# Optimization experiments

Hardware: AMD Instinct MI355X
Metric: run time of the kernel (lower is better)

## Reference

```python
import jax, jax.numpy as jnp
import numpy as np

R = 64  # all tensor-ring ranks equal

def setup_inputs() -> dict:
    key = jax.random.key(0)
    k1, k2, k3 = jax.random.split(key, 3)
    B, T, N, M, C = 512, 64, 512, 64, 100
    # xavier-uniform-ish scale for weights (gain=init_value=1.0)
    s_sh = float(np.sqrt(6.0 / (R * N + R)))
    s_la = float(np.sqrt(6.0 / (C * R * M + R)))
    return {
        "tensor": jax.random.normal(k1, (B, T, N), dtype=jnp.float32),
        "W_shared": jax.random.uniform(k2, (R, N, R), dtype=jnp.float32, minval=-s_sh, maxval=s_sh),
        "W_last": jax.random.uniform(k3, (C, R, M, R), dtype=jnp.float32, minval=-s_la, maxval=s_la),
    }

def reference(tensor, W_shared, W_last):
    B = tensor.shape[0]
    xt = jnp.transpose(tensor, (1, 0, 2))  # [T, B, N]
    state0 = jnp.ones((R, B, R), dtype=tensor.dtype)  # [r1, B, r2]
    # per-step: x = einsum('bj,rbi->rbji'); state = einsum('ijk,rbji->rbk')
    # == einsum('bj,rbi,ijk->rbk'); factored to avoid the [r,b,n,r] intermediate
    def step(state, x_t):
        bik = jnp.einsum('bj,ijk->bik', x_t, W_shared)   # [B, r2, r3]
        new = jnp.einsum('rbi,bik->rbk', state, bik)     # [r1, B, r3]
        return new, None
    state, _ = jax.lax.scan(step, state0, xt)
    # last kernel with pad_input = ones(B, m):
    # einsum('cijk,rbji->cbrk') with x[r,b,j,i]=state[r,b,i] == sum over j of W_last
    W_sum = jnp.sum(W_last, axis=2)                      # [C, r2, r_last]
    state = jnp.einsum('cik,rbi->cbrk', W_sum, state)    # [C, B, r1, r_last]
    # trace over the last two (square) rank dims
    out = jnp.einsum('cbrr->cb', state)                  # [C, B]
    return out
```

## Files before the change

kernel.cpp:

```cpp
#include <hip/hip_runtime.h>
#include <hip/hip_fp16.h>


typedef _Float16 f16;
typedef __attribute__((ext_vector_type(8))) _Float16 f16x8;
typedef __attribute__((ext_vector_type(2))) _Float16 f16x2;
typedef __attribute__((ext_vector_type(4))) float f32x4;

#define GLDS16(g, l)                                                      \
    __builtin_amdgcn_global_load_lds(                                     \
        (const __attribute__((address_space(1))) void*)(g),               \
        (__attribute__((address_space(3))) void*)(l), 16, 0, 0)

#define BARRIER() asm volatile("s_barrier" ::: "memory")
#define VMCNT(n) asm volatile("s_waitcnt vmcnt(" #n ")" ::: "memory")
#define WAVE_LDS_FENCE()                                                  \
    do {                                                                  \
        asm volatile("s_waitcnt lgkmcnt(0)" ::: "memory");                \
        __builtin_amdgcn_sched_barrier(0);                                \
    } while (0)

__global__ __launch_bounds__(256) void k_usum(const float* __restrict__ Wl,
                                              float* __restrict__ u) {
    int ci = blockIdx.x;
    const float4* p = (const float4*)(Wl + (size_t)ci * 4096);
    int tid = threadIdx.x;
    float s = 0.f;
#pragma unroll
    for (int q = 0; q < 4; ++q) {
        float4 v = p[tid + 256 * q];
        s += v.x + v.y + v.z + v.w;
    }
    __shared__ float red[256];
    red[tid] = s;
    __syncthreads();
    if (tid < 128) red[tid] += red[tid + 128];
    __syncthreads();
    if (tid < 64) {
        float x = red[tid] + red[tid + 64];
#pragma unroll
        for (int off = 32; off > 0; off >>= 1) x += __shfl_down(x, off, 64);
        if (tid == 0) u[ci] = x;
    }
}

__global__ __launch_bounds__(256) void k_prep(const float* __restrict__ tensor,
                                              const float* __restrict__ Wsh,
                                              const float* __restrict__ Wl,
                                              f16* __restrict__ Af16,
                                              f16* __restrict__ Btw,
                                              float* __restrict__ u) {
    __shared__ float red[256];
    int blk = blockIdx.x;
    int tid = threadIdx.x;
    if (blk < 8192) {
        int idx = blk * 256 + tid;
        const float4* p = (const float4*)tensor + (size_t)idx * 2;
        float4 v0 = p[0], v1 = p[1];
        f16x8 h;
        h[0] = (f16)v0.x; h[1] = (f16)v0.y; h[2] = (f16)v0.z; h[3] = (f16)v0.w;
        h[4] = (f16)v1.x; h[5] = (f16)v1.y; h[6] = (f16)v1.z; h[7] = (f16)v1.w;
        *(f16x8*)(Af16 + (size_t)idx * 8) = h;
    } else if (blk < 12288) {
        int o = (blk - 8192) * 256 + tid;
        int col = o >> 8;
        int j = (o & 255) << 1;
        int k = col >> 6, i = col & 63;
        const float* src = Wsh + ((size_t)i * 512 + j) * 64 + k;
        f16x2 pk;
        pk[0] = (f16)src[0];
        pk[1] = (f16)src[64];
        *(f16x2*)(Btw + (size_t)col * 512 + j) = pk;
    } else {
        int ci = blk - 12288;
        const float4* p = (const float4*)(Wl + (size_t)ci * 4096);
        float s = 0.f;
#pragma unroll
        for (int q = 0; q < 4; ++q) {
            float4 v = p[tid + 256 * q];
            s += v.x + v.y + v.z + v.w;
        }
        red[tid] = s;
        __syncthreads();
        if (tid < 128) red[tid] += red[tid + 128];
        __syncthreads();
        if (tid < 64) {
            float x = red[tid] + red[tid + 64];
#pragma unroll
            for (int off = 32; off > 0; off >>= 1) x += __shfl_down(x, off, 64);
            if (tid == 0) u[ci] = x;
        }
    }
}

#define STAGE_A(qq, ha, ktv) do {                                             \
    _Pragma("unroll") for (int u_ = 0; u_ < 2; ++u_) {                        \
        int idx_ = (wid * 2 + u_) * 64 + lane;                                \
        int r_ = idx_ >> 3;                                                   \
        int ls_ = (idx_ & 7) ^ (r_ & 7);                                      \
        const f16* g_ = A + (size_t)(m0 + (ha) * 128 + r_) * 512              \
                          + (ktv) * 64 + ls_ * 8;                             \
        char* l_ = smem + (qq) * 65536 + (ha) * 16384 + (wid * 2 + u_) * 1024;\
        GLDS16(g_, l_);                                                       \
    } } while (0)

#define STAGE_B(qq, hb, ktv) do {                                             \
    _Pragma("unroll") for (int u_ = 0; u_ < 2; ++u_) {                        \
        int idx_ = (wid * 2 + u_) * 64 + lane;                                \
        int r_ = idx_ >> 3;                                                   \
        int ls_ = (idx_ & 7) ^ (r_ & 7);                                      \
        const f16* g_ = Bt + (size_t)(n0 + (hb) * 128 + r_) * 512             \
                           + (ktv) * 64 + ls_ * 8;                            \
        char* l_ = smem + (qq) * 65536 + 32768 + (hb) * 16384                 \
                        + (wid * 2 + u_) * 1024;                              \
        GLDS16(g_, l_);                                                       \
    } } while (0)

#define RD_A(ha, ktv) do {                                                    \
    _Pragma("unroll") for (int mf_ = 0; mf_ < 4; ++mf_)                       \
    _Pragma("unroll") for (int kq_ = 0; kq_ < 2; ++kq_) {                     \
        int ra_ = wr * 64 + mf_ * 16 + (lane & 15);                           \
        int off_ = ((ra_ << 7) + kq_ * 64 + ((lane >> 4) << 4))               \
                   ^ ((ra_ & 7) << 4);                                        \
        a[mf_][kq_] = *(const f16x8*)(smem + ((ktv) & 1) * 65536              \
                                      + (ha) * 16384 + off_);                 \
    } } while (0)

#define RD_B(hb, ktv, breg) do {                                              \
    _Pragma("unroll") for (int nf_ = 0; nf_ < 2; ++nf_)                       \
    _Pragma("unroll") for (int kq_ = 0; kq_ < 2; ++kq_) {                     \
        int rb_ = wc * 32 + nf_ * 16 + (lane & 15);                           \
        int off_ = ((rb_ << 7) + kq_ * 64 + ((lane >> 4) << 4))               \
                   ^ ((rb_ & 7) << 4);                                        \
        breg[nf_][kq_] = *(const f16x8*)(smem + ((ktv) & 1) * 65536           \
                                         + 32768 + (hb) * 16384 + off_);      \
    } } while (0)

#define MFMA_Q(qa_, qb_, breg) do {                                           \
    __builtin_amdgcn_s_setprio(1);                                            \
    _Pragma("unroll") for (int mf_ = 0; mf_ < 4; ++mf_)                       \
    _Pragma("unroll") for (int nf_ = 0; nf_ < 2; ++nf_)                       \
    _Pragma("unroll") for (int kq_ = 0; kq_ < 2; ++kq_)                       \
        acc[qa_][qb_][mf_][nf_] = __builtin_amdgcn_mfma_f32_16x16x32_f16(     \
            a[mf_][kq_], breg[nf_][kq_], acc[qa_][qb_][mf_][nf_], 0, 0, 0);   \
    __builtin_amdgcn_s_setprio(0);                                            \
    } while (0)

__global__ __launch_bounds__(512) void k_gemm_256(const f16* __restrict__ A,
                                                  const f16* __restrict__ Bt,
                                                  __half* __restrict__ outp) {
    extern __shared__ char smem[];
    const int tid = threadIdx.x;
    const int lane = tid & 63;
    const int wid = tid >> 6;
    int lin = blockIdx.x;
    int swz = (lin & 7) * 256 + (lin >> 3);
    const int n0 = (swz & 15) * 256;
    const int m0 = (swz >> 4) * 256;
    const int wr = wid >> 2, wc = wid & 3;

    f32x4 acc[2][2][4][2];
#pragma unroll
    for (int x = 0; x < 2; ++x)
#pragma unroll
        for (int y = 0; y < 2; ++y)
#pragma unroll
            for (int z = 0; z < 4; ++z)
#pragma unroll
                for (int w = 0; w < 2; ++w) acc[x][y][z][w] = (f32x4)0.f;

    f16x8 a[4][2], b0[2][2], b1[2][2];

    STAGE_A(0, 0, 0);
    STAGE_B(0, 0, 0);
    STAGE_B(0, 1, 0);
    STAGE_A(0, 1, 0);
    STAGE_A(1, 0, 1);
    STAGE_B(1, 0, 1);
    STAGE_B(1, 1, 1);

    for (int kt = 0; kt < 6; ++kt) {
        VMCNT(6);
        BARRIER();
        RD_A(0, kt);
        RD_B(0, kt, b0);
        STAGE_A((kt + 1) & 1, 1, kt + 1);
        MFMA_Q(0, 0, b0);
        BARRIER();
        RD_B(1, kt, b1);
        MFMA_Q(0, 1, b1);
        BARRIER();
        RD_A(1, kt);
        STAGE_A(kt & 1, 0, kt + 2);
        STAGE_B(kt & 1, 0, kt + 2);
        MFMA_Q(1, 0, b0);
        BARRIER();
        STAGE_B(kt & 1, 1, kt + 2);
        MFMA_Q(1, 1, b1);
        BARRIER();
    }
    {
        VMCNT(6);
        BARRIER();
        RD_A(0, 6);
        RD_B(0, 6, b0);
        STAGE_A(1, 1, 7);
        MFMA_Q(0, 0, b0);
        BARRIER();
        RD_B(1, 6, b1);
        MFMA_Q(0, 1, b1);
        BARRIER();
        RD_A(1, 6);
        MFMA_Q(1, 0, b0);
        BARRIER();
        MFMA_Q(1, 1, b1);
        BARRIER();
    }
    {
        VMCNT(0);
        BARRIER();
        RD_A(0, 7);
        RD_B(0, 7, b0);
        MFMA_Q(0, 0, b0);
        BARRIER();
        RD_B(1, 7, b1);
        MFMA_Q(0, 1, b1);
        BARRIER();
        RD_A(1, 7);
        MFMA_Q(1, 0, b0);
        BARRIER();
        MFMA_Q(1, 1, b1);
        BARRIER();
    }

    __half* Cs = (__half*)smem;
#pragma unroll
    for (int qa = 0; qa < 2; ++qa)
#pragma unroll
        for (int qb = 0; qb < 2; ++qb)
#pragma unroll
            for (int mf = 0; mf < 4; ++mf)
#pragma unroll
                for (int nf = 0; nf < 2; ++nf)
#pragma unroll
                    for (int j = 0; j < 4; ++j) {
                        int row = qa * 128 + wr * 64 + mf * 16 + ((lane >> 4) << 2) + j;
                        int col = qb * 128 + wc * 32 + nf * 16 + (lane & 15);
                        Cs[row * 256 + col] = __float2half(acc[qa][qb][mf][nf][j]);
                    }
    BARRIER();
#pragma unroll
    for (int it = 0; it < 16; ++it) {
        int idx = it * 512 + tid;
        int r = idx >> 5, seg = idx & 31;
        __builtin_nontemporal_store(
            *(const f32x4*)(Cs + r * 256 + seg * 8),
            (f32x4*)(outp + (size_t)(m0 + r) * 4096 + n0 + seg * 8));
    }
}

#define BM 128
#define BN 64
#define BK 32
__global__ __launch_bounds__(256) void k_gemm(const float* __restrict__ A,
                                              const float* __restrict__ W,
                                              __half* __restrict__ out,
                                              int a_off, int a_stride) {
    __shared__ float As[BK * BM];
    __shared__ float Bs[BK * BN];
    int i0 = blockIdx.x;
    int m0 = blockIdx.y * BM;
    int tid = threadIdx.x;
    int tx = tid & 15, ty = tid >> 4;
    float acc[8][4];
#pragma unroll
    for (int q = 0; q < 8; ++q)
#pragma unroll
        for (int c = 0; c < 4; ++c) acc[q][c] = 0.f;
    const float* wbase = W + (size_t)i0 * 32768;
    for (int j0 = 0; j0 < 512; j0 += BK) {
        {
            int c4 = tid & 7;
            int r = tid >> 3;
#pragma unroll
            for (int p = 0; p < 4; ++p) {
                int row = r + 32 * p;
                float4 v = *(const float4*)(A + (size_t)a_off +
                                            (size_t)(m0 + row) * a_stride + j0 + 4 * c4);
                As[(4 * c4 + 0) * BM + row] = v.x;
                As[(4 * c4 + 1) * BM + row] = v.y;
                As[(4 * c4 + 2) * BM + row] = v.z;
                As[(4 * c4 + 3) * BM + row] = v.w;
            }
            const float4* src = (const float4*)(wbase + (size_t)j0 * 64);
            float4* dst = (float4*)Bs;
            dst[tid] = src[tid];
            dst[tid + 256] = src[tid + 256];
        }
        __syncthreads();
#pragma unroll
        for (int kk = 0; kk < BK; ++kk) {
            float bv[4], av[8];
#pragma unroll
            for (int c = 0; c < 4; ++c) bv[c] = Bs[kk * BN + 4 * tx + c];
#pragma unroll
            for (int q = 0; q < 8; ++q) av[q] = As[kk * BM + 8 * ty + q];
#pragma unroll
            for (int q = 0; q < 8; ++q)
#pragma unroll
                for (int c = 0; c < 4; ++c) acc[q][c] += av[q] * bv[c];
        }
        __syncthreads();
    }
#pragma unroll
    for (int q = 0; q < 8; ++q) {
        int m = m0 + 8 * ty + q;
        __half* o = out + (size_t)m * 4096 + i0 * 64 + 4 * tx;
#pragma unroll
        for (int c = 0; c < 4; ++c) o[c] = __float2half(acc[q][c]);
    }
}

__global__ __launch_bounds__(128) void k_scan_t(const __half* __restrict__ bik,
                                                const float* __restrict__ u,
                                                float* __restrict__ out) {
    __shared__ float vsh[2][64];
    const int tid = threadIdx.x;
    const int wid = tid >> 6;
    const int k = tid & 63;
    const int b = blockIdx.x * 2 + wid;
    float* vs = vsh[wid];
    const f16* row = (const f16*)bik + ((size_t)b * 64) * 4096 + k * 64;

    vs[k] = 1.0f;
    f16x8 A0[8], A1[8];
#pragma unroll
    for (int q = 0; q < 8; ++q) A0[q] = *(const f16x8*)(row + q * 8);
#pragma unroll
    for (int q = 0; q < 8; ++q) A1[q] = *(const f16x8*)(row + 4096 + q * 8);
    WAVE_LDS_FENCE();

#define SCAN_T_STEP(BUF, tnext) do {                                          \
    float s0 = 0.f, s1 = 0.f, s2 = 0.f, s3 = 0.f;                             \
    _Pragma("unroll") for (int q_ = 0; q_ < 8; q_ += 4) {                     \
        _Pragma("unroll") for (int e_ = 0; e_ < 8; ++e_) {                    \
            s0 += vs[(q_ + 0) * 8 + e_] * (float)BUF[q_ + 0][e_];             \
            s1 += vs[(q_ + 1) * 8 + e_] * (float)BUF[q_ + 1][e_];             \
            s2 += vs[(q_ + 2) * 8 + e_] * (float)BUF[q_ + 2][e_];             \
            s3 += vs[(q_ + 3) * 8 + e_] * (float)BUF[q_ + 3][e_];             \
        }                                                                     \
    }                                                                         \
    if ((tnext) < 64) {                                                       \
        const f16* r_ = row + (size_t)(tnext) * 4096;                         \
        _Pragma("unroll") for (int q_ = 0; q_ < 8; ++q_)                      \
            BUF[q_] = *(const f16x8*)(r_ + q_ * 8);                           \
    }                                                                         \
    vs[k] = (s0 + s1) + (s2 + s3);                                            \
    WAVE_LDS_FENCE();                                                         \
    } while (0)

    for (int t = 0; t < 64; t += 2) {
        SCAN_T_STEP(A0, t + 2);
        SCAN_T_STEP(A1, t + 3);
    }

    for (int c = k; c < 100; c += 64) {
        const float* uc = u + c * 64;
        float s = 0.f;
#pragma unroll 8
        for (int i = 0; i < 64; ++i) s += uc[i] * vs[i];
        out[c * 512 + b] = s;
    }
}

__global__ __launch_bounds__(256) void k_scan(const __half* __restrict__ bik,
                                              const float* __restrict__ u,
                                              float* __restrict__ out) {
    __shared__ char sm[2][8192];
    __shared__ float vsh[64];
    __shared__ float part[256];
    int b = blockIdx.x;
    int tid = threadIdx.x;
    int k = tid & 63, grp = tid >> 6;
    const int lane = tid & 63;
    const int wid = tid >> 6;
    if (tid < 64) vsh[tid] = 1.0f;
    const char* base = (const char*)(bik + (size_t)b * 64 * 4096);
#pragma unroll
    for (int u_ = 0; u_ < 2; ++u_) {
        const char* g = base + (wid * 2 + u_) * 1024 + lane * 16;
        GLDS16(g, &sm[0][0] + (wid * 2 + u_) * 1024);
    }
    for (int t = 0; t < 64; ++t) {
        VMCNT(0);
        __syncthreads();
        if (t < 63) {
            const char* gb = base + (size_t)(t + 1) * 8192;
#pragma unroll
            for (int u_ = 0; u_ < 2; ++u_) {
                const char* g = gb + (wid * 2 + u_) * 1024 + lane * 16;
                GLDS16(g, &sm[(t + 1) & 1][0] + (wid * 2 + u_) * 1024);
            }
        }
        const __half* Mt = (const __half*)&sm[t & 1][0];
        float s = 0.f;
#pragma unroll
        for (int q = 0; q < 16; ++q) {
            int i = grp * 16 + q;
            s += vsh[i] * __half2float(Mt[i * 64 + k]);
        }
        part[tid] = s;
        __syncthreads();
        if (tid < 64) vsh[k] = part[k] + part[64 + k] + part[128 + k] + part[192 + k];
        __syncthreads();
    }
    if (tid < 100) {
        const float* uc = u + tid * 64;
        float s = 0.f;
#pragma unroll 8
        for (int i = 0; i < 64; ++i) s += uc[i] * vsh[i];
        out[tid * 512 + b] = s;
    }
}

__global__ __launch_bounds__(256) void k_update(const __half* __restrict__ Mt,
                                                const float* __restrict__ vin,
                                                float* __restrict__ vout, int first) {
    int o = blockIdx.x * 256 + threadIdx.x;
    int b = o >> 6, k = o & 63;
    const __half* m = Mt + (size_t)b * 4096;
    float s = 0.f;
    if (first) {
#pragma unroll 8
        for (int i = 0; i < 64; ++i) s += __half2float(m[i * 64 + k]);
    } else {
        const float* v = vin + (size_t)b * 64;
#pragma unroll 8
        for (int i = 0; i < 64; ++i) s += v[i] * __half2float(m[i * 64 + k]);
    }
    vout[o] = s;
}

__global__ __launch_bounds__(256) void k_final(const float* __restrict__ u,
                                               const float* __restrict__ v,
                                               float* __restrict__ out) {
    int o = blockIdx.x * 256 + threadIdx.x;
    int c = o >> 9, b = o & 511;
    const float* uc = u + c * 64;
    const float* vb = v + (size_t)b * 64;
    float s = 0.f;
#pragma unroll 8
    for (int i = 0; i < 64; ++i) s += uc[i] * vb[i];
    out[o] = s;
}

extern "C" void kernel_launch(void* const* d_in, const int* in_sizes, int n_in,
                              void* d_out, int out_size, void* d_ws, size_t ws_size,
                              hipStream_t stream) {
    const float* tensor = (const float*)d_in[0];
    const float* Wsh = (const float*)d_in[1];
    const float* Wl = (const float*)d_in[2];
    float* out = (float*)d_out;
    char* ws = (char*)d_ws;

    const size_t bik_bytes = (size_t)32768 * 4096 * sizeof(__half);
    const size_t fast_bytes = bik_bytes + (512u << 10) + ((size_t)16777216 * 2) + ((size_t)4096 * 512 * 2);

    if (ws_size >= fast_bytes) {
        __half* bik = (__half*)ws;
        float* u = (float*)(ws + bik_bytes);
        f16* Af16 = (f16*)(ws + bik_bytes + (512u << 10));
        f16* Btw = Af16 + (size_t)16777216;

        k_prep<<<18688, 256, 0, stream>>>(tensor, Wsh, Wl, Af16, Btw, u);
        (void)hipFuncSetAttribute((const void*)k_gemm_256,
                                  hipFuncAttributeMaxDynamicSharedMemorySize, 131072);
        k_gemm_256<<<2048, 512, 131072, stream>>>(Af16, Btw, bik);
        k_scan_t<<<256, 128, 0, stream>>>(bik, u, out);
    } else if (ws_size >= bik_bytes + (2u << 20)) {
        __half* bik = (__half*)ws;
        float* u = (float*)(ws + bik_bytes);

        k_usum<<<6400, 256, 0, stream>>>(Wl, u);
        dim3 g(64, 256);
        k_gemm<<<g, 256, 0, stream>>>(tensor, Wsh, bik, 0, 512);
        k_scan<<<512, 256, 0, stream>>>(bik, u, out);
    } else {
        __half* bikt = (__half*)ws;
        float* u = (float*)(ws + (size_t)(4 << 20));
        float* v0 = (float*)(ws + (size_t)(4 << 20) + (64 << 10));
        float* v1 = v0 + 32768;

        k_usum<<<6400, 256, 0, stream>>>(Wl, u);
        for (int t = 0; t < 64; ++t) {
            dim3 g(64, 4);
            k_gemm<<<g, 256, 0, stream>>>(tensor, Wsh, bikt, t * 512, 32768);
            float* vin = (t & 1) ? v0 : v1;
            float* vout = (t & 1) ? v1 : v0;
            k_update<<<128, 256, 0, stream>>>(bikt, (t == 0) ? v0 : vin, vout, t == 0);
        }
        k_final<<<200, 256, 0, stream>>>(u, v1, out);
    }
}
```

Before: 251.1 us.

## Restructure GEMM main loop into a ping-pong register pipeline with finer staging

The 256x256 f16 GEMM tile loop is rewritten so A fragments are double-buffered in registers (a0/a1). The next k-step's LDS reads are issued before the current MFMA quadrant finishes, and global-to-LDS staging is interleaved per half-tile with finer vmcnt waits. The goal is to hide LDS and global load latency behind MFMA work. It also adds launch_bounds(512,2) to request two blocks per CU, which caps registers per thread and may cause spills given the extra A register buffer.

```diff
diff --git a/kernel.cpp b/kernel.cpp
--- a/kernel.cpp
+++ b/kernel.cpp
@@ -93,6 +93,7 @@
     }
 }
 
+
 #define STAGE_A(qq, ha, ktv) do {                                             \
     _Pragma("unroll") for (int u_ = 0; u_ < 2; ++u_) {                        \
         int idx_ = (wid * 2 + u_) * 64 + lane;                                \
@@ -116,14 +117,14 @@
         GLDS16(g_, l_);                                                       \
     } } while (0)
 
-#define RD_A(ha, ktv) do {                                                    \
+#define RD_A(ha, ktv, areg) do {                                              \
     _Pragma("unroll") for (int mf_ = 0; mf_ < 4; ++mf_)                       \
     _Pragma("unroll") for (int kq_ = 0; kq_ < 2; ++kq_) {                     \
         int ra_ = wr * 64 + mf_ * 16 + (lane & 15);                           \
         int off_ = ((ra_ << 7) + kq_ * 64 + ((lane >> 4) << 4))               \
                    ^ ((ra_ & 7) << 4);                                        \
-        a[mf_][kq_] = *(const f16x8*)(smem + ((ktv) & 1) * 65536              \
-                                      + (ha) * 16384 + off_);                 \
+        areg[mf_][kq_] = *(const f16x8*)(smem + ((ktv) & 1) * 65536           \
+                                         + (ha) * 16384 + off_);              \
     } } while (0)
 
 #define RD_B(hb, ktv, breg) do {                                              \
@@ -136,19 +137,19 @@
                                          + 32768 + (hb) * 16384 + off_);      \
     } } while (0)
 
-#define MFMA_Q(qa_, qb_, breg) do {                                           \
+#define MFMA_Q(qa_, qb_, areg, breg) do {                                     \
     __builtin_amdgcn_s_setprio(1);                                            \
     _Pragma("unroll") for (int mf_ = 0; mf_ < 4; ++mf_)                       \
     _Pragma("unroll") for (int nf_ = 0; nf_ < 2; ++nf_)                       \
     _Pragma("unroll") for (int kq_ = 0; kq_ < 2; ++kq_)                       \
         acc[qa_][qb_][mf_][nf_] = __builtin_amdgcn_mfma_f32_16x16x32_f16(     \
-            a[mf_][kq_], breg[nf_][kq_], acc[qa_][qb_][mf_][nf_], 0, 0, 0);   \
+            areg[mf_][kq_], breg[nf_][kq_], acc[qa_][qb_][mf_][nf_], 0, 0, 0);\
     __builtin_amdgcn_s_setprio(0);                                            \
     } while (0)
 
-__global__ __launch_bounds__(512) void k_gemm_256(const f16* __restrict__ A,
-                                                  const f16* __restrict__ Bt,
-                                                  __half* __restrict__ outp) {
+__global__ __launch_bounds__(512, 2) void k_gemm_256(const f16* __restrict__ A,
+                                                     const f16* __restrict__ Bt,
+                                                     __half* __restrict__ outp) {
     extern __shared__ char smem[];
     const int tid = threadIdx.x;
     const int lane = tid & 63;
@@ -161,15 +162,15 @@
 
     f32x4 acc[2][2][4][2];
 #pragma unroll
-    for (int x = 0; x < 2; ++x)
-#pragma unroll
-        for (int y = 0; y < 2; ++y)
-#pragma unroll
-            for (int z = 0; z < 4; ++z)
-#pragma unroll
-                for (int w = 0; w < 2; ++w) acc[x][y][z][w] = (f32x4)0.f;
-
-    f16x8 a[4][2], b0[2][2], b1[2][2];
+    for (int xx = 0; xx < 2; ++xx)
+#pragma unroll
+        for (int yy = 0; yy < 2; ++yy)
+#pragma unroll
+            for (int zz = 0; zz < 4; ++zz)
+#pragma unroll
+                for (int ww = 0; ww < 2; ++ww) acc[xx][yy][zz][ww] = (f32x4)0.f;
+
+    f16x8 a0[4][2], a1[4][2], b0[2][2], b1[2][2];
 
     STAGE_A(0, 0, 0);
     STAGE_B(0, 0, 0);
@@ -177,61 +178,64 @@
     STAGE_A(0, 1, 0);
     STAGE_A(1, 0, 1);
     STAGE_B(1, 0, 1);
+    VMCNT(8);
+    BARRIER();
+    RD_A(0, 0, a0);
+    RD_B(0, 0, b0);
+    VMCNT(4);
+    BARRIER();
+
+    RD_B(1, 0, b1);
+    MFMA_Q(0, 0, a0, b0);
+    BARRIER();
+    RD_A(1, 0, a1);
+    MFMA_Q(0, 1, a0, b1);
+    BARRIER();
     STAGE_B(1, 1, 1);
-
-    for (int kt = 0; kt < 6; ++kt) {
-        VMCNT(6);
+    STAGE_A(1, 1, 1);
+    MFMA_Q(1, 0, a1, b0);
+    VMCNT(4);
+    BARRIER();
+    RD_A(0, 1, a0);
+    RD_B(0, 1, b0);
+    MFMA_Q(1, 1, a1, b1);
+    VMCNT(2);
+    BARRIER();
+
+#pragma unroll
+    for (int kt = 1; kt < 7; ++kt) {
+        RD_B(1, kt, b1);
+        STAGE_A((kt + 1) & 1, 0, kt + 1);
+        STAGE_B((kt + 1) & 1, 0, kt + 1);
+        MFMA_Q(0, 0, a0, b0);
+        VMCNT(4);
         BARRIER();
-        RD_A(0, kt);
-        RD_B(0, kt, b0);
+        RD_A(1, kt, a1);
+        MFMA_Q(0, 1, a0, b1);
+        BARRIER();
+        STAGE_B((kt + 1) & 1, 1, kt + 1);
         STAGE_A((kt + 1) & 1, 1, kt + 1);
-        MFMA_Q(0, 0, b0);
+        MFMA_Q(1, 0, a1, b0);
+        VMCNT(4);
         BARRIER();
-        RD_B(1, kt, b1);
-        MFMA_Q(0, 1, b1);
+        RD_A(0, kt + 1, a0);
+        RD_B(0, kt + 1, b0);
+        MFMA_Q(1, 1, a1, b1);
+        VMCNT(2);
         BARRIER();
-        RD_A(1, kt);
-        STAGE_A(kt & 1, 0, kt + 2);
-        STAGE_B(kt & 1, 0, kt + 2);
-        MFMA_Q(1, 0, b0);
-        BARRIER();
-        STAGE_B(kt & 1, 1, kt + 2);
-        MFMA_Q(1, 1, b1);
-        BARRIER();
-    }
-    {
-        VMCNT(6);
-        BARRIER();
-        RD_A(0, 6);
-        RD_B(0, 6, b0);
-        STAGE_A(1, 1, 7);
-        MFMA_Q(0, 0, b0);
-        BARRIER();
-        RD_B(1, 6, b1);
-        MFMA_Q(0, 1, b1);
-        BARRIER();
-        RD_A(1, 6);
-        MFMA_Q(1, 0, b0);
-        BARRIER();
-        MFMA_Q(1, 1, b1);
-        BARRIER();
-    }
-    {
-        VMCNT(0);
-        BARRIER();
-        RD_A(0, 7);
-        RD_B(0, 7, b0);
-        MFMA_Q(0, 0, b0);
-        BARRIER();
-        RD_B(1, 7, b1);
-        MFMA_Q(0, 1, b1);
-        BARRIER();
-        RD_A(1, 7);
-        MFMA_Q(1, 0, b0);
-        BARRIER();
-        MFMA_Q(1, 1, b1);
-        BARRIER();
-    }
+    }
+
+    RD_B(1, 7, b1);
+    MFMA_Q(0, 0, a0, b0);
+    VMCNT(0);
+    BARRIER();
+    RD_A(1, 7, a1);
+    MFMA_Q(0, 1, a0, b1);
+    BARRIER();
+    MFMA_Q(1, 0, a1, b0);
+    BARRIER();
+    MFMA_Q(1, 1, a1, b1);
+    BARRIER();
 
     __half* Cs = (__half*)smem;
 #pragma unroll
```

After: 358.8 us. 42.9% more time.
